# Optimization experiments

Measured on AMD Instinct MI355X. Metric: run time of the kernel, lower is better.

The kernel has to match this reference:

```python
import jax, jax.numpy as jnp
import numpy as np

EPS = 1e-5

def inorm(x):
    # instance norm over time (last) axis; torch.std is unbiased (ddof=1)
    m = jnp.mean(x, axis=-1, keepdims=True)
    s = jnp.sqrt(jnp.var(x, axis=-1, ddof=1, keepdims=True))
    return (x - m) / (s + EPS)

def tinorm(x):
    # time-wise instance norm: normalize over channel axis (dim=1)
    m = jnp.mean(x, axis=1, keepdims=True)
    s = jnp.sqrt(jnp.var(x, axis=1, ddof=1, keepdims=True))
    return (x - m) / (s + EPS)

def adaptive_norm(src, trg, wq, wk, wv, norm_fn):
    # src, trg: [B,C,T]; wq/wk/wv: [out,in] as in nn.Linear
    temp = src.shape[1] ** 0.5
    q = jnp.einsum('bct,oc->bto', norm_fn(src), wq)        # [B,Ts,C]
    k = jnp.einsum('bct,oc->bto', norm_fn(trg), wk)        # [B,Tt,C]
    v = jnp.einsum('bct,oc->bto', trg, wv)                 # [B,Tt,C]
    attn = jax.nn.softmax(jnp.einsum('bsc,btc->bst', q / temp, k), axis=-1)
    mean = jnp.einsum('bst,btc->bsc', attn, v)             # attn-weighted mean
    var = jax.nn.relu(jnp.einsum('bst,btc->bsc', attn, v * v) - mean * mean)
    mean_c = jnp.mean(mean, axis=1)[:, :, None]            # [B,C,1]
    std_c = jnp.sqrt(jnp.mean(var, axis=1))[:, :, None]    # [B,C,1]
    return std_c * inorm(src) + mean_c

def sap(x, w, b):
    # self-attention pooling over axis 1; x: [B,N,C], w: [C], b: [1]
    a = jax.nn.softmax(jnp.einsum('bnc,c->bn', x, w) + b, axis=-1)
    return jnp.einsum('bnc,bn->bc', x, a)

def setup_inputs():
    key = jax.random.key(0)
    ks = jax.random.split(key, 24)
    B, C, Ts, Tt, S = 4, 512, 2048, 2048, 2048
    sc = 1.0 / np.sqrt(C).astype(np.float32)
    return {
        'src': jax.random.normal(ks[0], (B, C, Ts), jnp.float32),
        'trg': jax.random.normal(ks[1], (B, C, Tt), jnp.float32),
        'means': jax.random.normal(ks[2], (B, S, C), jnp.float32),
        'stds': jax.random.uniform(ks[3], (B, S, C), jnp.float32),
        'wq_t': jax.random.normal(ks[4], (C, C), jnp.float32) * sc,
        'wk_t': jax.random.normal(ks[5], (C, C), jnp.float32) * sc,
        'wv_t': jax.random.normal(ks[6], (C, C), jnp.float32) * sc,
        'wq_c': jax.random.normal(ks[7], (C, C), jnp.float32) * sc,
        'wk_c': jax.random.normal(ks[8], (C, C), jnp.float32) * sc,
        'wv_c': jax.random.normal(ks[9], (C, C), jnp.float32) * sc,
        'conv1_w': jax.random.normal(ks[10], (C, 2 * C), jnp.float32) * sc,
        'conv1_b': jax.random.normal(ks[11], (C,), jnp.float32) * 0.02,
        'conv2_w': jax.random.normal(ks[12], (C, C, 3), jnp.float32) * sc,
        'bn_g': jax.random.uniform(ks[13], (C,), jnp.float32, 0.5, 1.5),
        'bn_b': jax.random.normal(ks[14], (C,), jnp.float32) * 0.05,
        'bn_m': jax.random.normal(ks[15], (C,), jnp.float32) * 0.1,
        'bn_v': jax.random.uniform(ks[16], (C,), jnp.float32, 0.5, 1.5),
        'msap_w': jax.random.normal(ks[17], (C,), jnp.float32) * sc,
        'msap_b': jax.random.normal(ks[18], (1,), jnp.float32) * 0.02,
        'ssap_w': jax.random.normal(ks[19], (C,), jnp.float32) * sc,
        'ssap_b': jax.random.normal(ks[20], (1,), jnp.float32) * 0.02,
    }

def reference(src, trg, means, stds, wq_t, wk_t, wv_t, wq_c, wk_c, wv_c,
              conv1_w, conv1_b, conv2_w, bn_g, bn_b, bn_m, bn_v,
              msap_w, msap_b, ssap_w, ssap_b):
    src1 = adaptive_norm(src, trg, wq_t, wk_t, wv_t, tinorm)   # TAN
    src2 = adaptive_norm(src, trg, wq_c, wk_c, wv_c, inorm)    # CAN
    x = jnp.concatenate([src1, src2], axis=1)                  # [B,2C,T]
    # conv1: kernel_size=1 -> pointwise GEMM
    x = jnp.einsum('bct,oc->bot', x, conv1_w) + conv1_b[None, :, None]
    # conv2: Conv1d(k=3, pad=1, bias=False) + BatchNorm1d(eval) + ReLU
    x = jax.lax.conv_general_dilated(x, conv2_w, (1,), 'SAME',
                                     dimension_numbers=('NCH', 'OIH', 'NCH'))
    x = (x - bn_m[None, :, None]) * jax.lax.rsqrt(bn_v[None, :, None] + EPS)
    x = x * bn_g[None, :, None] + bn_b[None, :, None]
    x = jax.nn.relu(x)
    # GLAN
    mean = sap(means, msap_w, msap_b)[:, :, None]              # [B,C,1]
    std = sap(stds, ssap_w, ssap_b)[:, :, None]                # [B,C,1]
    return inorm(x) * std + mean
```

## Files before the change

### kernel.cpp

```cpp
#include <hip/hip_runtime.h>
#include <cstdint>
#include <cstddef>

#define B_ 4
#define C_ 512
#define T_ 2048
#define S_ 2048
#define EPSF 1e-5f

typedef __bf16 bf16;
typedef __attribute__((ext_vector_type(8))) __bf16 bf16x8;
typedef __attribute__((ext_vector_type(4))) float f32x4;

__device__ __forceinline__ bf16 f2b(float f){ return (bf16)f; }
__device__ __forceinline__ float b2f(bf16 h){ return (float)h; }

__device__ __forceinline__ void gl_lds16(const void* g, void* l){
  __builtin_amdgcn_global_load_lds((__attribute__((address_space(1))) void*)(g),
                                   (__attribute__((address_space(3))) void*)(l), 16, 0, 0);
}

__device__ __forceinline__ float wave_sum(float v){
#pragma unroll
  for (int o = 32; o; o >>= 1) v += __shfl_xor(v, o, 64);
  return v;
}
__device__ __forceinline__ float wave_max(float v){
#pragma unroll
  for (int o = 32; o; o >>= 1) v = fmaxf(v, __shfl_xor(v, o, 64));
  return v;
}

template<int EPI, int TNW>
__global__ void __launch_bounds__(256) gemm_nt(
    const bf16* __restrict__ A, const bf16* __restrict__ Bm, void* __restrict__ Cout,
    int K, int lda, int ldb, int ldc,
    long long sA, long long sB, long long sC, long long sCb,
    int zdivA, int zmodB, float scale,
    const float* __restrict__ rs, const float* __restrict__ rsh,
    const float* __restrict__ cbias,
    float* __restrict__ osum, float* __restrict__ osum2, long long sRs,
    float* __restrict__ ocol)
{
  constexpr int TN = TNW*32;
  __shared__ alignas(16) bf16 lA[128*64];
  __shared__ alignas(16) bf16 lB[TN*64];
  __shared__ float redcs[EPI == 3 ? 32*68 : 1];
  const int tid = threadIdx.x;
  const int z = blockIdx.z;
  const bf16* Ab = A + (long long)(z / zdivA) * sA;
  const bf16* Bb = Bm + (long long)(z % zmodB) * sB;
  const int m0 = blockIdx.y*128, n0 = blockIdx.x*TN;
  const int lane = tid & 63, wvi = tid >> 6;
  const int wm = wvi >> 1, wn = wvi & 1;

  f32x4 acc[4][TNW] = {};

  const int lrow = tid >> 3;
  const int lcol = ((tid ^ lrow) & 7) * 8;
  const bf16* pa = Ab + (long long)(m0 + lrow)*lda + lcol;
  const bf16* pb = Bb + (long long)(n0 + lrow)*ldb + lcol;
  char* sa = (char*)lA + tid*16;
  char* sb = (char*)lB + tid*16;

  const int csg = tid >> 3, csph = tid & 7;
  float linv4[4];
  if (EPI == 3) {
#pragma unroll
    for (int rr = 0; rr < 4; ++rr)
      linv4[rr] = 1.f / rs[(long long)z*sRs + (m0 + csg*4 + rr)];
  }

  for (int k0 = 0; k0 < K; k0 += 64) {
#pragma unroll
    for (int it = 0; it < 4; ++it)
      gl_lds16(pa + (long long)it*32*lda + k0, sa + it*4096);
#pragma unroll
    for (int it = 0; it < TNW; ++it)
      gl_lds16(pb + (long long)it*32*ldb + k0, sb + it*4096);
    __syncthreads();
#pragma unroll
    for (int ks = 0; ks < 2; ++ks) {
      const int kq = ks*4 + (lane >> 4);
      bf16x8 af[4], bfr[TNW];
#pragma unroll
      for (int mt = 0; mt < 4; ++mt) {
        int r = wm*64 + mt*16 + (lane & 15);
        af[mt] = *(const bf16x8*)&lA[r*64 + ((kq ^ (r & 7))*8)];
      }
#pragma unroll
      for (int nt = 0; nt < TNW; ++nt) {
        int r = wn*(TNW*16) + nt*16 + (lane & 15);
        bfr[nt] = *(const bf16x8*)&lB[r*64 + ((kq ^ (r & 7))*8)];
      }
#pragma unroll
      for (int mt = 0; mt < 4; ++mt)
#pragma unroll
        for (int nt = 0; nt < TNW; ++nt)
          acc[mt][nt] = __builtin_amdgcn_mfma_f32_16x16x32_bf16(af[mt], bfr[nt], acc[mt][nt], 0, 0, 0);
    }
    bool own = false;
    if (EPI == 3) {
      own = ((k0 >> 6) & 3) == (int)blockIdx.x;
      if (own) {
        float part[8] = {0.f,0.f,0.f,0.f,0.f,0.f,0.f,0.f};
#pragma unroll
        for (int rr = 0; rr < 4; ++rr) {
          const int r = csg*4 + rr;
          bf16x8 v = *(const bf16x8*)&lA[r*64 + ((csph ^ (r & 7))*8)];
          const float li = linv4[rr];
#pragma unroll
          for (int j = 0; j < 8; ++j) part[j] += b2f(v[j]) * li;
        }
#pragma unroll
        for (int j = 0; j < 8; ++j) redcs[csg*68 + csph*8 + j] = part[j];
      }
    }
    __syncthreads();
    if (EPI == 3) {
      if (own && tid < 64) {
        float s = 0.f;
#pragma unroll
        for (int g2 = 0; g2 < 32; ++g2) s += redcs[g2*68 + tid];
        atomicAdd(&ocol[(long long)z*lda + k0 + tid], s);
      }
    }
  }

  if (EPI == 3) {
    float* red1 = (float*)lA;
    float* red2 = red1 + 4*TNW*16;
    const int cr = (lane >> 4)*4;
    float linv[4][4];
#pragma unroll
    for (int mt = 0; mt < 4; ++mt)
#pragma unroll
      for (int i = 0; i < 4; ++i)
        linv[mt][i] = 1.f / rs[(long long)z*sRs + (m0 + wm*64 + mt*16 + cr + i)];
    float s1[TNW], s2[TNW];
#pragma unroll
    for (int nt = 0; nt < TNW; ++nt) {
      s1[nt] = 0.f; s2[nt] = 0.f;
#pragma unroll
      for (int mt = 0; mt < 4; ++mt)
#pragma unroll
        for (int i = 0; i < 4; ++i) {
          float v = acc[mt][nt][i] * linv[mt][i];
          s1[nt] += v; s2[nt] += v*v;
        }
      s1[nt] += __shfl_xor(s1[nt], 16, 64);
      s1[nt] += __shfl_xor(s1[nt], 32, 64);
      s2[nt] += __shfl_xor(s2[nt], 16, 64);
      s2[nt] += __shfl_xor(s2[nt], 32, 64);
    }
    __syncthreads();
    if (lane < 16) {
#pragma unroll
      for (int nt = 0; nt < TNW; ++nt) {
        red1[(wvi*TNW + nt)*16 + lane] = s1[nt];
        red2[(wvi*TNW + nt)*16 + lane] = s2[nt];
      }
    }
    __syncthreads();
    if (tid < 2*TN) {
      const int which = tid >= TN;
      const int col = tid - which*TN;
      const int wn2 = col / (TNW*16), rem = col % (TNW*16);
      const float* rr = which ? red2 : red1;
      float v = rr[wn2*(TNW*16) + rem] + rr[(2+wn2)*(TNW*16) + rem];
      float* dst = which ? osum2 : osum;
      atomicAdd(&dst[sCb*z + n0 + col], v);
    }
    return;
  }

  const int cr = (lane >> 4)*4, cc = lane & 15;
#pragma unroll
  for (int mt = 0; mt < 4; ++mt) {
#pragma unroll
    for (int i = 0; i < 4; ++i) {
      const int mm = m0 + wm*64 + mt*16 + cr + i;
      float rsum = 0.f, rsum2 = 0.f;
#pragma unroll
      for (int nt = 0; nt < TNW; ++nt) {
        const int nn = n0 + wn*(TNW*16) + nt*16 + cc;
        float v = acc[mt][nt][i];
        const long long co = sC*z + (long long)mm*ldc + nn;
        if (EPI == 0) {
          v *= scale;
          if (cbias) v += cbias[sCb*z + nn];
          ((bf16*)Cout)[co] = f2b(v);
        } else if (EPI == 2) {
          v = fmaxf(v*rs[mm] + rsh[mm], 0.f);
          ((float*)Cout)[co] = v;
          rsum += v; rsum2 += v*v;
        } else if (EPI == 4) {
          v = __expf(v);
          ((bf16*)Cout)[co] = f2b(v);
          rsum += v;
        }
      }
      if (EPI == 2 || EPI == 4) {
        rsum += __shfl_xor(rsum, 1, 64); rsum += __shfl_xor(rsum, 2, 64);
        rsum += __shfl_xor(rsum, 4, 64); rsum += __shfl_xor(rsum, 8, 64);
        if (EPI == 2) {
          rsum2 += __shfl_xor(rsum2, 1, 64); rsum2 += __shfl_xor(rsum2, 2, 64);
          rsum2 += __shfl_xor(rsum2, 4, 64); rsum2 += __shfl_xor(rsum2, 8, 64);
        }
        if (cc == 0) {
          atomicAdd(&osum[(long long)z*sRs + mm], rsum);
          if (EPI == 2) atomicAdd(&osum2[(long long)z*sRs + mm], rsum2);
        }
      }
    }
  }
}

__global__ void __launch_bounds__(512, 2) qk_exp_k(
    const bf16* __restrict__ Q, const bf16* __restrict__ Km,
    bf16* __restrict__ P, float* __restrict__ lsum)
{
  __shared__ alignas(16) char lds[131072];
  const int tid = threadIdx.x;
  const int lane = tid & 63, wvi = tid >> 6;
  const int wm = wvi >> 2, wn = wvi & 3;
  const int l15 = lane & 15, lq = lane >> 4;
  const int swz = l15 & 7;

  const int t0i = blockIdx.x * 2;
  const int z   = t0i >> 6;
  const int by  = (t0i >> 3) & 7;
  const int bx0 = t0i & 7;

  f32x4 acc[8][4] = {};

  const int lr = tid >> 3;
  const int lc = ((tid ^ lr) & 7) * 8;
  const bf16* pa  = Q  + (long long)z*(2048LL*512) + (long long)(by*256 + lr)*512 + lc;
  const bf16* pb0 = Km + (long long)z*(2048LL*512) + (long long)(bx0*256 + lr)*512 + lc;

  auto STAGE = [&](int b, int u) {
    char* da = (char*)lds + b*65536 + tid*16;
    const int kt = u & 7;
    const bf16* ga = pa + kt*64;
    const bf16* gb = pb0 + ((u >> 3) ? 256*512 : 0) + kt*64;
#pragma unroll
    for (int it = 0; it < 4; ++it) gl_lds16(ga + (long long)it*64*512, da + it*8192);
#pragma unroll
    for (int it = 0; it < 4; ++it) gl_lds16(gb + (long long)it*64*512, da + 32768 + it*8192);
  };

  auto EPI = [&](int rep) {
    const int m0 = by*256, n0 = (bx0 + rep)*256;
    const long long zT = (long long)z * 2048;
    bf16* Cb = P + zT * 2048;
    float* lrw = lsum + zT;
    const int cr = lq * 4;
#pragma unroll
    for (int mt = 0; mt < 8; ++mt) {
#pragma unroll
      for (int i = 0; i < 4; ++i) {
        const int mm = m0 + wm*128 + mt*16 + cr + i;
        float rsum = 0.f;
#pragma unroll
        for (int nt = 0; nt < 4; ++nt) {
          const int nn = n0 + wn*64 + nt*16 + l15;
          float v = __expf(acc[mt][nt][i]);
          Cb[(long long)mm*2048 + nn] = f2b(v);
          rsum += v;
        }
        rsum += __shfl_xor(rsum, 1, 64); rsum += __shfl_xor(rsum, 2, 64);
        rsum += __shfl_xor(rsum, 4, 64); rsum += __shfl_xor(rsum, 8, 64);
        if (l15 == 0) atomicAdd(&lrw[mm], rsum);
      }
    }
#pragma unroll
    for (int mt = 0; mt < 8; ++mt)
#pragma unroll
      for (int nt = 0; nt < 4; ++nt)
        acc[mt][nt] = f32x4{0.f, 0.f, 0.f, 0.f};
  };

  STAGE(0, 0);
  for (int u = 0; u < 16; ++u) {
    const int cur = u & 1;
    if (u < 15) {
      STAGE(cur ^ 1, u + 1);
      asm volatile("s_waitcnt vmcnt(8)" ::: "memory");
    } else {
      asm volatile("s_waitcnt vmcnt(0)" ::: "memory");
    }
    __builtin_amdgcn_s_barrier();

    const bf16* lA = (const bf16*)(lds + cur*65536);
    const bf16* lB = lA + 16384;

    bf16x8 af[4], bfr[4];
#pragma unroll
    for (int half = 0; half < 4; ++half) {
      const int ks = half >> 1, mg = (half & 1) * 4;
      const int kq = ks*4 + lq;
      const int ko = (kq ^ swz) * 8;
      if ((half & 1) == 0) {
#pragma unroll
        for (int nt = 0; nt < 4; ++nt)
          bfr[nt] = *(const bf16x8*)&lB[(wn*64 + nt*16 + l15)*64 + ko];
      }
#pragma unroll
      for (int mt = 0; mt < 4; ++mt)
        af[mt] = *(const bf16x8*)&lA[(wm*128 + (mg + mt)*16 + l15)*64 + ko];
      __builtin_amdgcn_s_barrier();
      __builtin_amdgcn_s_setprio(1);
#pragma unroll
      for (int mt = 0; mt < 4; ++mt)
#pragma unroll
        for (int nt = 0; nt < 4; ++nt)
          acc[mg + mt][nt] = __builtin_amdgcn_mfma_f32_16x16x32_bf16(
              af[mt], bfr[nt], acc[mg + mt][nt], 0, 0, 0);
      __builtin_amdgcn_s_setprio(0);
      __builtin_amdgcn_s_barrier();
    }
    if (u == 7) EPI(0);
  }
  EPI(1);
}

__global__ void __launch_bounds__(256) row_stats_k(const float* __restrict__ X1,
    const float* __restrict__ X2, float* __restrict__ Mo, float* __restrict__ So, int n1)
{
  __shared__ float r1[4], r2[4];
  const int row = blockIdx.x;
  const float* x = (row < n1) ? X1 + (long long)row*T_ : X2 + (long long)(row-n1)*T_;
  float s1 = 0.f, s2 = 0.f;
  for (int i = threadIdx.x; i < T_; i += 256){ float v = x[i]; s1 += v; s2 += v*v; }
  s1 = wave_sum(s1); s2 = wave_sum(s2);
  const int lane = threadIdx.x & 63, w = threadIdx.x >> 6;
  if (!lane){ r1[w] = s1; r2[w] = s2; }
  __syncthreads();
  if (threadIdx.x == 0){
    s1 = r1[0]+r1[1]+r1[2]+r1[3];
    s2 = r2[0]+r2[1]+r2[2]+r2[3];
    float m = s1 * (1.f/T_);
    float var = (s2 - s1*m) * (1.f/(T_-1));
    Mo[row] = m; So[row] = sqrtf(fmaxf(var, 0.f));
  }
}

__global__ void __launch_bounds__(256) col_stats_k(const float* __restrict__ src,
    const float* __restrict__ trg, float* __restrict__ Mo, float* __restrict__ So)
{
  __shared__ float r1[4][64], r2[4][64];
  const int z = blockIdx.y, t0 = blockIdx.x*64;
  const float* X = (z < B_) ? src : trg;
  const int b = z & (B_-1);
  const int tl = threadIdx.x & 63, cg = threadIdx.x >> 6;
  float s1 = 0.f, s2 = 0.f;
  for (int c = cg; c < C_; c += 4) {
    float v = X[((long long)b*C_ + c)*T_ + t0 + tl];
    s1 += v; s2 += v*v;
  }
  r1[cg][tl] = s1; r2[cg][tl] = s2;
  __syncthreads();
  if (cg == 0) {
    s1 = r1[0][tl]+r1[1][tl]+r1[2][tl]+r1[3][tl];
    s2 = r2[0][tl]+r2[1][tl]+r2[2][tl]+r2[3][tl];
    float m = s1 * (1.f/C_);
    float var = (s2 - s1*m) * (1.f/(C_-1));
    Mo[z*T_ + t0 + tl] = m;
    So[z*T_ + t0 + tl] = sqrtf(fmaxf(var, 0.f));
  }
}

__global__ void __launch_bounds__(256) transform_k(const float* __restrict__ src,
    const float* __restrict__ trg,
    const float* __restrict__ tnm, const float* __restrict__ tns,
    const float* __restrict__ inm, const float* __restrict__ ins,
    bf16* __restrict__ NSt, bf16* __restrict__ NSc,
    bf16* __restrict__ NTt, bf16* __restrict__ NTc, bf16* __restrict__ TTr)
{
  __shared__ float tile[32][33];
  const int z = blockIdx.z, t0 = blockIdx.x*32, c0 = blockIdx.y*32;
  const int is_t = z >= B_, b = z & (B_-1);
  const float* X = is_t ? trg : src;
  const int tx = threadIdx.x, ty = threadIdx.y;
#pragma unroll
  for (int r = 0; r < 4; ++r) {
    int ci = ty + r*8;
    tile[ci][tx] = X[((long long)b*C_ + c0 + ci)*T_ + t0 + tx];
  }
  __syncthreads();
#pragma unroll
  for (int r = 0; r < 4; ++r) {
    int tj = ty + r*8, ci = tx;
    float v = tile[ci][tj];
    int gt = t0 + tj, gc = c0 + ci;
    float a = (v - tnm[z*T_ + gt]) / (tns[z*T_ + gt] + EPSF);
    float d = (v - inm[z*C_ + gc]) / (ins[z*C_ + gc] + EPSF);
    long long o = ((long long)b*T_ + gt)*C_ + gc;
    if (is_t) { NTt[o] = f2b(a); NTc[o] = f2b(d); TTr[o] = f2b(v); }
    else      { NSt[o] = f2b(a); NSc[o] = f2b(d); }
  }
}

__global__ void __launch_bounds__(256) softmax_row_k(const float* __restrict__ X, float* __restrict__ O)
{
  __shared__ float red[4];
  const long long row = blockIdx.x;
  const float* x = X + row*T_ + threadIdx.x*8;
  float v[8];
  f32x4 a0 = *(const f32x4*)x;
  f32x4 a1 = *(const f32x4*)(x + 4);
#pragma unroll
  for (int j = 0; j < 4; ++j){ v[j] = a0[j]; v[4+j] = a1[j]; }
  float m = -3.4e38f;
#pragma unroll
  for (int j = 0; j < 8; ++j) m = fmaxf(m, v[j]);
  m = wave_max(m);
  const int lane = threadIdx.x & 63, w = threadIdx.x >> 6;
  if (!lane) red[w] = m;
  __syncthreads();
  m = fmaxf(fmaxf(red[0], red[1]), fmaxf(red[2], red[3]));
  __syncthreads();
  float s = 0.f;
#pragma unroll
  for (int j = 0; j < 8; ++j){ v[j] = __expf(v[j] - m); s += v[j]; }
  s = wave_sum(s);
  if (!lane) red[w] = s;
  __syncthreads();
  s = red[0]+red[1]+red[2]+red[3];
  const float inv = 1.f/s;
  float* o = O + row*T_ + threadIdx.x*8;
#pragma unroll
  for (int j = 0; j < 8; ++j) o[j] = v[j]*inv;
}

__global__ void __launch_bounds__(256) vv_fin_k(const float* __restrict__ cs,
    const bf16* __restrict__ VT, const float* __restrict__ msum,
    const float* __restrict__ m2sum, float* __restrict__ meanc, float* __restrict__ stdc)
{
  __shared__ float r1[4];
  const int c = blockIdx.x, z = blockIdx.y;
  const bf16* vr = VT + ((long long)z*C_ + c)*T_;
  const float* w = cs + z*T_;
  float a = 0.f;
  for (int t = threadIdx.x; t < T_; t += 256){ float v = b2f(vr[t]); a += w[t]*v*v; }
  a = wave_sum(a);
  const int lane = threadIdx.x & 63, wq = threadIdx.x >> 6;
  if (!lane) r1[wq] = a;
  __syncthreads();
  if (threadIdx.x == 0){
    a = r1[0]+r1[1]+r1[2]+r1[3];
    const int idx = z*C_ + c;
    meanc[idx] = msum[idx] * (1.f/S_);
    float var = (a - m2sum[idx]) * (1.f/S_);
    stdc[idx] = sqrtf(fmaxf(var, 0.f));
  }
}

__global__ void __launch_bounds__(256) weff_k(const float* __restrict__ w1,
    const float* __restrict__ b1, const float* __restrict__ sdt, const float* __restrict__ sdc,
    const float* __restrict__ mct, const float* __restrict__ mcc,
    bf16* __restrict__ Weff, float* __restrict__ beff)
{
  __shared__ float r1[4];
  const int o = blockIdx.x, b = blockIdx.y;
  float accb = 0.f;
  for (int c = threadIdx.x; c < C_; c += 256) {
    float wa = w1[o*2*C_ + c], wb = w1[o*2*C_ + C_ + c];
    Weff[((long long)(b*C_ + o))*C_ + c] = f2b(wa*sdt[b*C_+c] + wb*sdc[b*C_+c]);
    accb += wa*mct[b*C_+c] + wb*mcc[b*C_+c];
  }
  accb = wave_sum(accb);
  const int lane = threadIdx.x & 63, w = threadIdx.x >> 6;
  if (!lane) r1[w] = accb;
  __syncthreads();
  if (threadIdx.x == 0) beff[b*C_ + o] = b1[o] + r1[0]+r1[1]+r1[2]+r1[3];
}

__global__ void __launch_bounds__(256) w2r_k(const float* __restrict__ w2,
    const float* __restrict__ g, const float* __restrict__ be,
    const float* __restrict__ mu, const float* __restrict__ va,
    bf16* __restrict__ W2r, float* __restrict__ bnsc, float* __restrict__ bnsh)
{
  const int o = blockIdx.x;
  for (int c = threadIdx.x; c < C_; c += 256)
#pragma unroll
    for (int dt = 0; dt < 3; ++dt)
      W2r[(long long)o*3*C_ + dt*C_ + c] = f2b(w2[((long long)o*C_ + c)*3 + dt]);
  if (threadIdx.x == 0) {
    float s = g[o] * rsqrtf(va[o] + EPSF);
    bnsc[o] = s;
    bnsh[o] = be[o] - mu[o]*s;
  }
}

__global__ void __launch_bounds__(256) cast6_k(const float* __restrict__ a0,
    const float* __restrict__ a1, const float* __restrict__ a2, const float* __restrict__ a3,
    const float* __restrict__ a4, const float* __restrict__ a5, bf16* __restrict__ o)
{
  const int i = blockIdx.x*256 + threadIdx.x;
  const int slot = i >> 18;
  const float* srcs[6] = {a0,a1,a2,a3,a4,a5};
  const float sc = (slot < 2) ? 0.044194173824159216f : 1.f;
  o[i] = f2b(srcs[slot][i & 262143] * sc);
}

__global__ void __launch_bounds__(256) zero_pad_k(bf16* __restrict__ x1p)
{
  const int i = blockIdx.x*256 + threadIdx.x;
  const int b = i >> 10, rem = i & 1023;
  const long long row = (rem >> 9) ? (T_+1) : 0;
  const int c = rem & (C_-1);
  x1p[((long long)b*(T_+2) + row)*C_ + c] = f2b(0.f);
}

__global__ void __launch_bounds__(256) zero_f32_k(float* __restrict__ p)
{
  p[blockIdx.x*256 + threadIdx.x] = 0.f;
}

__global__ void __launch_bounds__(256) sap_logit_k(const float* __restrict__ means,
    const float* __restrict__ stds, const float* __restrict__ mw, const float* __restrict__ sw,
    const float* __restrict__ mb, const float* __restrict__ sb, float* __restrict__ out)
{
  const int n = blockIdx.x*4 + (threadIdx.x >> 6);
  const int z = blockIdx.y;
  const int sel = z >= B_, b = z & (B_-1);
  const float* x = sel ? stds : means;
  const float* w = sel ? sw : mw;
  const int lane = threadIdx.x & 63;
  const float* p = x + ((long long)b*S_ + n)*C_;
  float a = 0.f;
  for (int c = lane; c < C_; c += 64) a += p[c]*w[c];
  a = wave_sum(a);
  if (!lane) out[z*S_ + n] = a + (sel ? sb[0] : mb[0]);
}

__global__ void __launch_bounds__(256) sap_wsum_k(const float* __restrict__ means,
    const float* __restrict__ stds, const float* __restrict__ a, float* __restrict__ out)
{
  const int c = blockIdx.x*256 + threadIdx.x;
  const int z = blockIdx.z;
  const int sel = z >= B_, b = z & (B_-1);
  const float* x = sel ? stds : means;
  const long long n0 = (long long)blockIdx.y*256;
  const float* p = x + ((long long)b*S_ + n0)*C_ + c;
  const float* aw = a + z*S_ + n0;
  float acc = 0.f;
  for (int n = 0; n < 256; ++n) acc += p[(long long)n*C_] * aw[n];
  atomicAdd(&out[z*C_ + c], acc);
}

__global__ void __launch_bounds__(256) final_k(const float* __restrict__ y,
    const float* __restrict__ ysum, const float* __restrict__ y2sum,
    const float* __restrict__ sapms, float* __restrict__ out)
{
  const long long i = (long long)(blockIdx.x*256 + threadIdx.x) * 4;
  const long long r = i >> 11;
  const float s1 = ysum[r], s2 = y2sum[r];
  const float m = s1 * (1.f/T_);
  const float var = (s2 - s1*m) * (1.f/(T_-1));
  const float inv = 1.f/(sqrtf(fmaxf(var, 0.f)) + EPSF);
  const float mn = sapms[r], sd = sapms[B_*C_ + r];
  const f32x4 v = *(const f32x4*)(y + i);
  f32x4 o;
#pragma unroll
  for (int j = 0; j < 4; ++j) o[j] = (v[j] - m)*inv*sd + mn;
  *(f32x4*)(out + i) = o;
}

extern "C" void kernel_launch(void* const* d_in, const int* in_sizes, int n_in,
                              void* d_out, int out_size, void* d_ws, size_t ws_size,
                              hipStream_t stream)
{
  (void)in_sizes; (void)n_in; (void)out_size; (void)ws_size;
  const float* src    = (const float*)d_in[0];
  const float* trg    = (const float*)d_in[1];
  const float* means  = (const float*)d_in[2];
  const float* stds   = (const float*)d_in[3];
  const float* conv1w = (const float*)d_in[10];
  const float* conv1b = (const float*)d_in[11];
  const float* conv2w = (const float*)d_in[12];
  const float* bn_g   = (const float*)d_in[13];
  const float* bn_b   = (const float*)d_in[14];
  const float* bn_m   = (const float*)d_in[15];
  const float* bn_v   = (const float*)d_in[16];
  const float* msap_w = (const float*)d_in[17];
  const float* msap_b = (const float*)d_in[18];
  const float* ssap_w = (const float*)d_in[19];
  const float* ssap_b = (const float*)d_in[20];

  const long long BTC = (long long)B_*T_*C_;

  char* p = (char*)d_ws;
  auto take = [&](size_t n)->char*{ char* r = p; p += (n + 255) & ~(size_t)255; return r; };

  bf16* NSc = (bf16*)take(BTC*2);
  bf16* P2  = (bf16*)take((size_t)2*B_*S_*T_*2);
  bf16* NSt = P2;
  bf16* NTc = P2 + BTC;
  bf16* NTt = P2 + 2*BTC;
  bf16* TTr = P2 + 3*BTC;
  bf16* QK4 = (bf16*)take((size_t)4*BTC*2);
  bf16* VT2 = (bf16*)take((size_t)2*BTC*2);
  bf16* WQb = (bf16*)take((size_t)6*C_*C_*2);
  bf16* Weff= (bf16*)take((size_t)B_*C_*C_*2);
  bf16* W2r = (bf16*)take((size_t)C_*3*C_*2);
  bf16* x1p = (bf16*)take((size_t)B_*(T_+2)*C_*2);
  float* y  = (float*)take((size_t)B_*C_*T_*4);
  float* colsum = (float*)take(2*B_*T_*4);
  float* msum   = (float*)take(2*B_*C_*4);
  float* m2sum  = (float*)take(2*B_*C_*4);
  float* sapms  = (float*)take(2*B_*C_*4);
  float* lrow   = (float*)take(2*B_*S_*4);
  float* ysum   = (float*)take(B_*C_*4);
  float* y2sum  = (float*)take(B_*C_*4);
  float* tnm = (float*)take(2*B_*T_*4);
  float* tns = (float*)take(2*B_*T_*4);
  float* inm = (float*)take(2*B_*C_*4);
  float* ins = (float*)take(2*B_*C_*4);
  float* meanc = (float*)take(2*B_*C_*4);
  float* stdc  = (float*)take(2*B_*C_*4);
  float* beff  = (float*)take(B_*C_*4);
  float* bnsc  = (float*)take(C_*4);
  float* bnsh  = (float*)take(C_*4);
  float* sapl  = (float*)take(2*B_*S_*4);
  float* sapa  = (float*)take(2*B_*S_*4);

  dim3 blk(256);

  cast6_k<<<6144, blk, 0, stream>>>((const float*)d_in[7], (const float*)d_in[4],
      (const float*)d_in[8], (const float*)d_in[5], (const float*)d_in[9],
      (const float*)d_in[6], WQb);
  w2r_k<<<C_, blk, 0, stream>>>(conv2w, bn_g, bn_b, bn_m, bn_v, W2r, bnsc, bnsh);
  row_stats_k<<<2*B_*C_, blk, 0, stream>>>(src, trg, inm, ins, B_*C_);
  col_stats_k<<<dim3(T_/64, 2*B_), blk, 0, stream>>>(src, trg, tnm, tns);
  transform_k<<<dim3(T_/32, C_/32, 2*B_), dim3(32,8), 0, stream>>>(src, trg,
      tnm, tns, inm, ins, NSt, NSc, NTt, NTc, TTr);
  zero_pad_k<<<16, blk, 0, stream>>>(x1p);
  zero_f32_k<<<192, blk, 0, stream>>>(colsum);

  gemm_nt<0,4><<<dim3(C_/128, (B_*T_)/128, 4), blk, 0, stream>>>(NSc, WQb, QK4,
      C_, C_, C_, C_, BTC, (long long)C_*C_, BTC, 0, 1, 8, 1.f,
      nullptr, nullptr, nullptr, nullptr, nullptr, 0, nullptr);
  gemm_nt<0,2><<<dim3(T_/64, C_/128, 8), blk, 0, stream>>>(WQb + (size_t)4*C_*C_, TTr, VT2,
      C_, C_, C_, T_, (long long)C_*C_, (long long)T_*C_, (long long)C_*T_, 0, 4, 4, 1.f,
      nullptr, nullptr, nullptr, nullptr, nullptr, 0, nullptr);
  qk_exp_k<<<dim3(256), dim3(512), 0, stream>>>(QK4, QK4 + 2*BTC, P2, lrow);
  gemm_nt<3,4><<<dim3(C_/128, S_/128, 8), blk, 0, stream>>>(P2, VT2, nullptr,
      T_, T_, T_, 0, (long long)S_*T_, (long long)C_*T_, 0, C_, 1, 8, 1.f,
      lrow, nullptr, nullptr, msum, m2sum, S_, colsum);
  vv_fin_k<<<dim3(C_, 2*B_), blk, 0, stream>>>(colsum, VT2, msum, m2sum, meanc, stdc);

  weff_k<<<dim3(C_, B_), blk, 0, stream>>>(conv1w, conv1b,
      stdc + B_*C_, stdc, meanc + B_*C_, meanc, Weff, beff);
  gemm_nt<0,2><<<dim3(C_/64, T_/128, B_), blk, 0, stream>>>(NSc, Weff, x1p + C_,
      C_, C_, C_, C_, (long long)T_*C_, (long long)C_*C_, (long long)(T_+2)*C_, C_,
      1, 8, 1.f, nullptr, nullptr, beff, nullptr, nullptr, 0, nullptr);
  gemm_nt<2,2><<<dim3(T_/64, C_/128, B_), blk, 0, stream>>>(W2r, x1p, y,
      3*C_, 3*C_, C_, T_, 0, (long long)(T_+2)*C_, (long long)C_*T_, 0,
      1, 8, 1.f, bnsc, bnsh, nullptr, ysum, y2sum, C_, nullptr);

  sap_logit_k<<<dim3(S_/4, 2*B_), blk, 0, stream>>>(means, stds, msap_w, ssap_w,
      msap_b, ssap_b, sapl);
  softmax_row_k<<<2*B_, blk, 0, stream>>>(sapl, sapa);
  sap_wsum_k<<<dim3(C_/256, S_/256, 2*B_), blk, 0, stream>>>(means, stds, sapa, sapms);

  final_k<<<4096, blk, 0, stream>>>(y, ysum, y2sum, sapms, (float*)d_out);
}
```

Measured before the change: 472.7 us.

## Fold normalization into QK weights and epilogue, transpose raw inputs once

The transform kernel now writes only the bf16 transpose of the raw src/trg instead of four normalized copies. The channel-wise instance norm is folded into per-batch effective Q/K weights and a bias (foldqk_k, weff_k). The time-wise norm is applied as a per-row scale and shift in a new GEMM epilogue (EPI 5). The aim is to cut the memory traffic of writing and reading several normalized activation tensors. In exchange the Q/K projection now runs per batch with 16 weight matrices, and the qk_exp kernel launches one tile per block instead of two, which adds launches and reloads.

```diff
diff --git a/kernel.cpp b/kernel.cpp
--- a/kernel.cpp
+++ b/kernel.cpp
@@ -198,6 +198,9 @@
           v = __expf(v);
           ((bf16*)Cout)[co] = f2b(v);
           rsum += v;
+        } else if (EPI == 5) {
+          v = v*rs[(long long)z*sRs + mm] + rsh[(long long)z*sRs + mm]*cbias[sCb*z + nn];
+          ((bf16*)Cout)[co] = f2b(v);
         }
       }
       if (EPI == 2 || EPI == 4) {
@@ -217,75 +220,42 @@
 }
 
 __global__ void __launch_bounds__(512, 2) qk_exp_k(
-    const bf16* __restrict__ Q, const bf16* __restrict__ Km,
-    bf16* __restrict__ P, float* __restrict__ lsum)
+    const bf16* __restrict__ QK, bf16* __restrict__ P, float* __restrict__ lsum)
 {
   __shared__ alignas(16) char lds[131072];
   const int tid = threadIdx.x;
+  const int z = blockIdx.z;
+  const int ph = z >> 2, b = z & 3;
+  const bf16* Qb = QK + (long long)(b*2 + ph) * (2048LL*512);
+  const bf16* Kb = QK + (long long)(8 + b*2 + ph) * (2048LL*512);
+  const int m0 = blockIdx.y * 256, n0 = blockIdx.x * 256;
   const int lane = tid & 63, wvi = tid >> 6;
   const int wm = wvi >> 2, wn = wvi & 3;
   const int l15 = lane & 15, lq = lane >> 4;
   const int swz = l15 & 7;
 
-  const int t0i = blockIdx.x * 2;
-  const int z   = t0i >> 6;
-  const int by  = (t0i >> 3) & 7;
-  const int bx0 = t0i & 7;
-
   f32x4 acc[8][4] = {};
 
   const int lr = tid >> 3;
   const int lc = ((tid ^ lr) & 7) * 8;
-  const bf16* pa  = Q  + (long long)z*(2048LL*512) + (long long)(by*256 + lr)*512 + lc;
-  const bf16* pb0 = Km + (long long)z*(2048LL*512) + (long long)(bx0*256 + lr)*512 + lc;
-
-  auto STAGE = [&](int b, int u) {
-    char* da = (char*)lds + b*65536 + tid*16;
-    const int kt = u & 7;
+  const bf16* pa = Qb + (long long)(m0 + lr)*512 + lc;
+  const bf16* pb = Kb + (long long)(n0 + lr)*512 + lc;
+
+  auto STAGE = [&](int bb, int kt) {
+    char* da = (char*)lds + bb*65536 + tid*16;
     const bf16* ga = pa + kt*64;
-    const bf16* gb = pb0 + ((u >> 3) ? 256*512 : 0) + kt*64;
-#pragma unroll
-    for (int it = 0; it < 4; ++it) gl_lds16(ga + (long long)it*64*512, da + it*8192);
-#pragma unroll
-    for (int it = 0; it < 4; ++it) gl_lds16(gb + (long long)it*64*512, da + 32768 + it*8192);
+    const bf16* gb = pb + kt*64;
+#pragma unroll
+    for (int it = 0; it < 4; ++it) gl_lds16(ga + it*64*512, da + it*8192);
+#pragma unroll
+    for (int it = 0; it < 4; ++it) gl_lds16(gb + it*64*512, da + 32768 + it*8192);
   };
 
-  auto EPI = [&](int rep) {
-    const int m0 = by*256, n0 = (bx0 + rep)*256;
-    const long long zT = (long long)z * 2048;
-    bf16* Cb = P + zT * 2048;
-    float* lrw = lsum + zT;
-    const int cr = lq * 4;
-#pragma unroll
-    for (int mt = 0; mt < 8; ++mt) {
-#pragma unroll
-      for (int i = 0; i < 4; ++i) {
-        const int mm = m0 + wm*128 + mt*16 + cr + i;
-        float rsum = 0.f;
-#pragma unroll
-        for (int nt = 0; nt < 4; ++nt) {
-          const int nn = n0 + wn*64 + nt*16 + l15;
-          float v = __expf(acc[mt][nt][i]);
-          Cb[(long long)mm*2048 + nn] = f2b(v);
-          rsum += v;
-        }
-        rsum += __shfl_xor(rsum, 1, 64); rsum += __shfl_xor(rsum, 2, 64);
-        rsum += __shfl_xor(rsum, 4, 64); rsum += __shfl_xor(rsum, 8, 64);
-        if (l15 == 0) atomicAdd(&lrw[mm], rsum);
-      }
-    }
-#pragma unroll
-    for (int mt = 0; mt < 8; ++mt)
-#pragma unroll
-      for (int nt = 0; nt < 4; ++nt)
-        acc[mt][nt] = f32x4{0.f, 0.f, 0.f, 0.f};
-  };
-
   STAGE(0, 0);
-  for (int u = 0; u < 16; ++u) {
-    const int cur = u & 1;
-    if (u < 15) {
-      STAGE(cur ^ 1, u + 1);
+  for (int kt = 0; kt < 8; ++kt) {
+    const int cur = kt & 1;
+    if (kt < 7) {
+      STAGE(cur ^ 1, kt + 1);
       asm volatile("s_waitcnt vmcnt(8)" ::: "memory");
     } else {
       asm volatile("s_waitcnt vmcnt(0)" ::: "memory");
@@ -320,9 +290,30 @@
       __builtin_amdgcn_s_setprio(0);
       __builtin_amdgcn_s_barrier();
     }
-    if (u == 7) EPI(0);
-  }
-  EPI(1);
+  }
+
+  const long long zT = (long long)z * 2048;
+  bf16* Cb = P + zT * 2048;
+  float* lrw = lsum + zT;
+  const int cr = lq * 4;
+#pragma unroll
+  for (int mt = 0; mt < 8; ++mt) {
+#pragma unroll
+    for (int i = 0; i < 4; ++i) {
+      const int mm = m0 + wm*128 + mt*16 + cr + i;
+      float rsum = 0.f;
+#pragma unroll
+      for (int nt = 0; nt < 4; ++nt) {
+        const int nn = n0 + wn*64 + nt*16 + l15;
+        float v = __expf(acc[mt][nt][i]);
+        Cb[(long long)mm*2048 + nn] = f2b(v);
+        rsum += v;
+      }
+      rsum += __shfl_xor(rsum, 1, 64); rsum += __shfl_xor(rsum, 2, 64);
+      rsum += __shfl_xor(rsum, 4, 64); rsum += __shfl_xor(rsum, 8, 64);
+      if (l15 == 0) atomicAdd(&lrw[mm], rsum);
+    }
+  }
 }
 
 __global__ void __launch_bounds__(256) row_stats_k(const float* __restrict__ X1,
@@ -372,11 +363,7 @@
 }
 
 __global__ void __launch_bounds__(256) transform_k(const float* __restrict__ src,
-    const float* __restrict__ trg,
-    const float* __restrict__ tnm, const float* __restrict__ tns,
-    const float* __restrict__ inm, const float* __restrict__ ins,
-    bf16* __restrict__ NSt, bf16* __restrict__ NSc,
-    bf16* __restrict__ NTt, bf16* __restrict__ NTc, bf16* __restrict__ TTr)
+    const float* __restrict__ trg, bf16* __restrict__ XT)
 {
   __shared__ float tile[32][33];
   const int z = blockIdx.z, t0 = blockIdx.x*32, c0 = blockIdx.y*32;
@@ -392,14 +379,58 @@
 #pragma unroll
   for (int r = 0; r < 4; ++r) {
     int tj = ty + r*8, ci = tx;
-    float v = tile[ci][tj];
-    int gt = t0 + tj, gc = c0 + ci;
-    float a = (v - tnm[z*T_ + gt]) / (tns[z*T_ + gt] + EPSF);
-    float d = (v - inm[z*C_ + gc]) / (ins[z*C_ + gc] + EPSF);
-    long long o = ((long long)b*T_ + gt)*C_ + gc;
-    if (is_t) { NTt[o] = f2b(a); NTc[o] = f2b(d); TTr[o] = f2b(v); }
-    else      { NSt[o] = f2b(a); NSc[o] = f2b(d); }
-  }
+    XT[((long long)z*T_ + t0 + tj)*C_ + c0 + ci] = f2b(tile[ci][tj]);
+  }
+}
+
+__global__ void __launch_bounds__(256) foldqk_k(
+    const float* __restrict__ wq_c, const float* __restrict__ wq_t,
+    const float* __restrict__ wk_c, const float* __restrict__ wk_t,
+    const float* __restrict__ inm, const float* __restrict__ ins,
+    bf16* __restrict__ W, float* __restrict__ cb)
+{
+  __shared__ float r1[4];
+  const int o = blockIdx.x, z = blockIdx.y;
+  const int side = z >> 3, b = (z >> 1) & 3, ph = z & 1;
+  const float* w = side ? (ph ? wk_t : wk_c) : (ph ? wq_t : wq_c);
+  const float sc = side ? 1.f : 0.044194173824159216f;
+  const int ofs = (side*B_ + b)*C_;
+  float acc = 0.f;
+  for (int c = threadIdx.x; c < C_; c += 256) {
+    float wv = w[o*C_ + c] * sc;
+    float out, contrib;
+    if (ph == 0) {
+      float ri = 1.f / (ins[ofs + c] + EPSF);
+      out = wv * ri;
+      contrib = -out * inm[ofs + c];
+    } else {
+      out = wv;
+      contrib = wv;
+    }
+    W[((long long)z*C_ + o)*C_ + c] = f2b(out);
+    acc += contrib;
+  }
+  acc = wave_sum(acc);
+  const int lane = threadIdx.x & 63, wq = threadIdx.x >> 6;
+  if (!lane) r1[wq] = acc;
+  __syncthreads();
+  if (threadIdx.x == 0) cb[z*C_ + o] = r1[0]+r1[1]+r1[2]+r1[3];
+}
+
+__global__ void __launch_bounds__(256) rsfill_k(
+    const float* __restrict__ tnm, const float* __restrict__ tns,
+    float* __restrict__ rsq, float* __restrict__ rshq)
+{
+  const int z = blockIdx.y, t = blockIdx.x*256 + threadIdx.x;
+  const int side = z >> 3, b = (z >> 1) & 3, ph = z & 1;
+  float rv, rh;
+  if (ph == 0) { rv = 1.f; rh = 1.f; }
+  else {
+    const int ofs = (side*B_ + b)*T_;
+    float r = 1.f / (tns[ofs + t] + EPSF);
+    rv = r; rh = -tnm[ofs + t] * r;
+  }
+  rsq[z*T_ + t] = rv; rshq[z*T_ + t] = rh;
 }
 
 __global__ void __launch_bounds__(256) softmax_row_k(const float* __restrict__ X, float* __restrict__ O)
@@ -460,15 +491,19 @@
 __global__ void __launch_bounds__(256) weff_k(const float* __restrict__ w1,
     const float* __restrict__ b1, const float* __restrict__ sdt, const float* __restrict__ sdc,
     const float* __restrict__ mct, const float* __restrict__ mcc,
+    const float* __restrict__ inm, const float* __restrict__ ins,
     bf16* __restrict__ Weff, float* __restrict__ beff)
 {
   __shared__ float r1[4];
   const int o = blockIdx.x, b = blockIdx.y;
+  const int ofs = b*C_;
   float accb = 0.f;
   for (int c = threadIdx.x; c < C_; c += 256) {
     float wa = w1[o*2*C_ + c], wb = w1[o*2*C_ + C_ + c];
-    Weff[((long long)(b*C_ + o))*C_ + c] = f2b(wa*sdt[b*C_+c] + wb*sdc[b*C_+c]);
-    accb += wa*mct[b*C_+c] + wb*mcc[b*C_+c];
+    float s = wa*sdt[b*C_+c] + wb*sdc[b*C_+c];
+    float w2 = s / (ins[ofs + c] + EPSF);
+    Weff[((long long)(b*C_ + o))*C_ + c] = f2b(w2);
+    accb += wa*mct[b*C_+c] + wb*mcc[b*C_+c] - w2*inm[ofs + c];
   }
   accb = wave_sum(accb);
   const int lane = threadIdx.x & 63, w = threadIdx.x >> 6;
@@ -494,15 +529,11 @@
   }
 }
 
-__global__ void __launch_bounds__(256) cast6_k(const float* __restrict__ a0,
-    const float* __restrict__ a1, const float* __restrict__ a2, const float* __restrict__ a3,
-    const float* __restrict__ a4, const float* __restrict__ a5, bf16* __restrict__ o)
+__global__ void __launch_bounds__(256) castv_k(const float* __restrict__ a0,
+    const float* __restrict__ a1, bf16* __restrict__ o)
 {
   const int i = blockIdx.x*256 + threadIdx.x;
-  const int slot = i >> 18;
-  const float* srcs[6] = {a0,a1,a2,a3,a4,a5};
-  const float sc = (slot < 2) ? 0.044194173824159216f : 1.f;
-  o[i] = f2b(srcs[slot][i & 262143] * sc);
+  o[i] = f2b(((i >> 18) ? a1 : a0)[i & 262143]);
 }
 
 __global__ void __launch_bounds__(256) zero_pad_k(bf16* __restrict__ x1p)
@@ -591,23 +622,21 @@
   const float* ssap_b = (const float*)d_in[20];
 
   const long long BTC = (long long)B_*T_*C_;
+  const long long TC  = (long long)T_*C_;
 
   char* p = (char*)d_ws;
   auto take = [&](size_t n)->char*{ char* r = p; p += (n + 255) & ~(size_t)255; return r; };
 
-  bf16* NSc = (bf16*)take(BTC*2);
   bf16* P2  = (bf16*)take((size_t)2*B_*S_*T_*2);
-  bf16* NSt = P2;
-  bf16* NTc = P2 + BTC;
-  bf16* NTt = P2 + 2*BTC;
-  bf16* TTr = P2 + 3*BTC;
-  bf16* QK4 = (bf16*)take((size_t)4*BTC*2);
+  bf16* QK4 = (bf16*)take((size_t)16*TC*2);
   bf16* VT2 = (bf16*)take((size_t)2*BTC*2);
-  bf16* WQb = (bf16*)take((size_t)6*C_*C_*2);
+  bf16* WQeff = (bf16*)take((size_t)16*C_*C_*2);
+  bf16* WVb = (bf16*)take((size_t)2*C_*C_*2);
   bf16* Weff= (bf16*)take((size_t)B_*C_*C_*2);
   bf16* W2r = (bf16*)take((size_t)C_*3*C_*2);
   bf16* x1p = (bf16*)take((size_t)B_*(T_+2)*C_*2);
   float* y  = (float*)take((size_t)B_*C_*T_*4);
+  bf16* XT  = (bf16*)y;
   float* colsum = (float*)take(2*B_*T_*4);
   float* msum   = (float*)take(2*B_*C_*4);
   float* m2sum  = (float*)take(2*B_*C_*4);
@@ -626,36 +655,39 @@
   float* bnsh  = (float*)take(C_*4);
   float* sapl  = (float*)take(2*B_*S_*4);
   float* sapa  = (float*)take(2*B_*S_*4);
+  float* cbq   = (float*)take(16*C_*4);
+  float* rsq   = (float*)take(16*T_*4);
+  float* rshq  = (float*)take(16*T_*4);
 
   dim3 blk(256);
 
-  cast6_k<<<6144, blk, 0, stream>>>((const float*)d_in[7], (const float*)d_in[4],
-      (const float*)d_in[8], (const float*)d_in[5], (const float*)d_in[9],
-      (const float*)d_in[6], WQb);
+  castv_k<<<2048, blk, 0, stream>>>((const float*)d_in[9], (const float*)d_in[6], WVb);
   w2r_k<<<C_, blk, 0, stream>>>(conv2w, bn_g, bn_b, bn_m, bn_v, W2r, bnsc, bnsh);
   row_stats_k<<<2*B_*C_, blk, 0, stream>>>(src, trg, inm, ins, B_*C_);
   col_stats_k<<<dim3(T_/64, 2*B_), blk, 0, stream>>>(src, trg, tnm, tns);
-  transform_k<<<dim3(T_/32, C_/32, 2*B_), dim3(32,8), 0, stream>>>(src, trg,
-      tnm, tns, inm, ins, NSt, NSc, NTt, NTc, TTr);
+  transform_k<<<dim3(T_/32, C_/32, 2*B_), dim3(32,8), 0, stream>>>(src, trg, XT);
+  foldqk_k<<<dim3(C_, 16), blk, 0, stream>>>((const float*)d_in[7], (const float*)d_in[4],
+      (const float*)d_in[8], (const float*)d_in[5], inm, ins, WQeff, cbq);
+  rsfill_k<<<dim3(T_/256, 16), blk, 0, stream>>>(tnm, tns, rsq, rshq);
   zero_pad_k<<<16, blk, 0, stream>>>(x1p);
   zero_f32_k<<<192, blk, 0, stream>>>(colsum);
 
-  gemm_nt<0,4><<<dim3(C_/128, (B_*T_)/128, 4), blk, 0, stream>>>(NSc, WQb, QK4,
-      C_, C_, C_, C_, BTC, (long long)C_*C_, BTC, 0, 1, 8, 1.f,
+  gemm_nt<5,4><<<dim3(C_/128, T_/128, 16), blk, 0, stream>>>(XT, WQeff, QK4,
+      C_, C_, C_, C_, TC, (long long)C_*C_, TC, C_,
+      2, 16, 1.f, rsq, rshq, cbq, nullptr, nullptr, T_, nullptr);
+  gemm_nt<0,2><<<dim3(T_/64, C_/128, 8), blk, 0, stream>>>(WVb, XT + 4*TC, VT2,
+      C_, C_, C_, T_, (long long)C_*C_, TC, (long long)C_*T_, 0, 4, 4, 1.f,
       nullptr, nullptr, nullptr, nullptr, nullptr, 0, nullptr);
-  gemm_nt<0,2><<<dim3(T_/64, C_/128, 8), blk, 0, stream>>>(WQb + (size_t)4*C_*C_, TTr, VT2,
-      C_, C_, C_, T_, (long long)C_*C_, (long long)T_*C_, (long long)C_*T_, 0, 4, 4, 1.f,
-      nullptr, nullptr, nullptr, nullptr, nullptr, 0, nullptr);
-  qk_exp_k<<<dim3(256), dim3(512), 0, stream>>>(QK4, QK4 + 2*BTC, P2, lrow);
+  qk_exp_k<<<dim3(T_/256, T_/256, 8), dim3(512), 0, stream>>>(QK4, P2, lrow);
   gemm_nt<3,4><<<dim3(C_/128, S_/128, 8), blk, 0, stream>>>(P2, VT2, nullptr,
       T_, T_, T_, 0, (long long)S_*T_, (long long)C_*T_, 0, C_, 1, 8, 1.f,
       lrow, nullptr, nullptr, msum, m2sum, S_, colsum);
   vv_fin_k<<<dim3(C_, 2*B_), blk, 0, stream>>>(colsum, VT2, msum, m2sum, meanc, stdc);
 
   weff_k<<<dim3(C_, B_), blk, 0, stream>>>(conv1w, conv1b,
-      stdc + B_*C_, stdc, meanc + B_*C_, meanc, Weff, beff);
-  gemm_nt<0,2><<<dim3(C_/64, T_/128, B_), blk, 0, stream>>>(NSc, Weff, x1p + C_,
-      C_, C_, C_, C_, (long long)T_*C_, (long long)C_*C_, (long long)(T_+2)*C_, C_,
+      stdc + B_*C_, stdc, meanc + B_*C_, meanc, inm, ins, Weff, beff);
+  gemm_nt<0,2><<<dim3(C_/64, T_/128, B_), blk, 0, stream>>>(XT, Weff, x1p + C_,
+      C_, C_, C_, C_, TC, (long long)C_*C_, (long long)(T_+2)*C_, C_,
       1, 8, 1.f, nullptr, nullptr, beff, nullptr, nullptr, 0, nullptr);
   gemm_nt<2,2><<<dim3(T_/64, C_/128, B_), blk, 0, stream>>>(W2r, x1p, y,
       3*C_, 3*C_, C_, T_, 0, (long long)(T_+2)*C_, (long long)C_*T_, 0,
```

Measured after the change: 458.3 us. 3.1% less time.
